# Performance work log

Hardware: AMD Instinct MI355X
Metric: run time of the kernel (lower is better)

## Reference

```python
import jax, jax.numpy as jnp
import numpy as np

B = 131072
N_X = 64
H = 512
LD = 8                      # latent_dim
N_THETA = 1 + LD + LD * (LD + 1) // 2   # 45
N_STEPS = 20
_IU = np.triu_indices(LD)   # static upper-tri index pairs for quadratic terms


def _layernorm(x, g, b, eps=1e-5):
    m = jnp.mean(x, axis=-1, keepdims=True)
    v = jnp.var(x, axis=-1, keepdims=True)
    return (x - m) * jax.lax.rsqrt(v + eps) * g + b


def _library(z):
    # Theta(z) = [1, z, upper-tri quadratic terms]  -> [B, N_THETA]
    ones = jnp.ones((z.shape[0], 1), z.dtype)
    quad = z[:, _IU[0]] * z[:, _IU[1]]
    return jnp.concatenate([ones, z, quad], axis=1)


def setup_inputs() -> dict:
    key = jax.random.key(0)
    ks = jax.random.split(key, 16)

    def W(k, fan_in, fan_out):
        # kaiming_normal (relu gain) as in the torch init
        return jax.random.normal(k, (fan_in, fan_out), jnp.float32) * np.sqrt(2.0 / fan_in)

    inp = {
        "x0_norm": jax.random.normal(ks[0], (B, N_X), jnp.float32),
        "log10_Dt_norm": jax.random.uniform(ks[1], (B, 1), jnp.float32),
        "Dt_mean": 0,
        "Dt_std": 1,
        # encoder: n_x -> 512 -> 512 -> latent (LN+SiLU between, final Tanh)
        "enc_W1": W(ks[2], N_X, H), "enc_b1": jnp.zeros((H,), jnp.float32),
        "enc_g1": jnp.ones((H,), jnp.float32), "enc_be1": jnp.zeros((H,), jnp.float32),
        "enc_W2": W(ks[3], H, H), "enc_b2": jnp.zeros((H,), jnp.float32),
        "enc_g2": jnp.ones((H,), jnp.float32), "enc_be2": jnp.zeros((H,), jnp.float32),
        "enc_W3": W(ks[4], H, LD), "enc_b3": jnp.zeros((LD,), jnp.float32),
        # decoder: latent -> 512 -> 512 -> n_x (LN+SiLU between, no final act)
        "dec_W1": W(ks[5], LD, H), "dec_b1": jnp.zeros((H,), jnp.float32),
        "dec_g1": jnp.ones((H,), jnp.float32), "dec_be1": jnp.zeros((H,), jnp.float32),
        "dec_W2": W(ks[6], H, H), "dec_b2": jnp.zeros((H,), jnp.float32),
        "dec_g2": jnp.ones((H,), jnp.float32), "dec_be2": jnp.zeros((H,), jnp.float32),
        "dec_W3": W(ks[7], H, N_X), "dec_b3": jnp.zeros((N_X,), jnp.float32),
        "Xi": 0.01 * jax.random.normal(ks[8], (N_THETA, LD), jnp.float32),
    }
    return inp


def reference(x0_norm, log10_Dt_norm, Dt_mean, Dt_std,
              enc_W1, enc_b1, enc_g1, enc_be1, enc_W2, enc_b2, enc_g2, enc_be2,
              enc_W3, enc_b3,
              dec_W1, dec_b1, dec_g1, dec_be1, dec_W2, dec_b2, dec_g2, dec_be2,
              dec_W3, dec_b3, Xi):
    # 1. encode: z0 = phi(x0)
    h = jax.nn.silu(_layernorm(x0_norm @ enc_W1 + enc_b1, enc_g1, enc_be1))
    h = jax.nn.silu(_layernorm(h @ enc_W2 + enc_b2, enc_g2, enc_be2))
    z0 = jnp.tanh(h @ enc_W3 + enc_b3)                       # [B, LD]

    # 2. Euler-integrate dz/dtau = Theta(z) Xi for N_STEPS fixed steps
    dt = log10_Dt_norm[:, :1] / N_STEPS                       # [B, 1]

    def step(z, _):
        zdot = _library(z) @ Xi                               # [B, LD]
        return z + zdot * dt, None

    z_t, _ = jax.lax.scan(step, z0, None, length=N_STEPS)

    # 3. decode: xhat = psi(z_t)
    h = jax.nn.silu(_layernorm(z_t @ dec_W1 + dec_b1, dec_g1, dec_be1))
    h = jax.nn.silu(_layernorm(h @ dec_W2 + dec_b2, dec_g2, dec_be2))
    xhat = h @ dec_W3 + dec_b3                                # [B, N_X]
    return xhat
```

## Files before the change

kernel.cpp:

```cpp
#include <hip/hip_runtime.h>
#include <hip/hip_bf16.h>
#include <math.h>

#define B_TOTAL 131072
#define NX 64
#define H 512
#define LD 8
#define NT 45
#define NSTEPS 20

#define NTH 512
#define BM 64
#define ASTR 520

#define OFF_EW1T 0
#define OFF_EW2T 32768
#define OFF_DW2T 294912
#define OFF_DW3T 557056
#define WS_ELEMS 589824
#define OFF_W3HI 589824
#define OFF_W3LO 598016
#define WS_ELEMS2 606208
#define OFF_DW1P 606208
#define WS_ELEMS3 622592
#define ZT_OFF_BYTES (WS_ELEMS3 * 2)
#define WS_NEW_BYTES (ZT_OFF_BYTES + (size_t)B_TOTAL * LD * 4)

typedef __attribute__((ext_vector_type(8))) short short8;
typedef __attribute__((ext_vector_type(4))) float f32x4;

__device__ __forceinline__ ushort f2bf(float f) {
    union { float f; uint u; } v; v.f = f;
    uint u = v.u;
    u += 0x7fff + ((u >> 16) & 1);
    return (ushort)(u >> 16);
}
__device__ __forceinline__ float bf2f(ushort s) {
    union { uint u; float f; } v; v.u = ((uint)s) << 16;
    return v.f;
}
__device__ __forceinline__ float silu_f(float v) {
    return v / (1.0f + __expf(-v));
}

__global__ void prep_weights(const float* __restrict__ eW1, const float* __restrict__ eW2,
                             const float* __restrict__ dW2, const float* __restrict__ dW3,
                             const float* __restrict__ eW3, const float* __restrict__ dW1,
                             short* __restrict__ ws) {
    const int id = blockIdx.x * 256 + threadIdx.x;
    if (id < OFF_EW2T) {
        const int kc = id >> 14, n = (id >> 5) & 511, kk = id & 31;
        ws[id] = (short)f2bf(eW1[(kc * 32 + kk) * H + n]);
    } else if (id < OFF_DW2T) {
        const int j = id - OFF_EW2T;
        const int kc = j >> 14, n = (j >> 5) & 511, kk = j & 31;
        ws[id] = (short)f2bf(eW2[(kc * 32 + kk) * H + n]);
    } else if (id < OFF_DW3T) {
        const int j = id - OFF_DW2T;
        const int kc = j >> 14, n = (j >> 5) & 511, kk = j & 31;
        ws[id] = (short)f2bf(dW2[(kc * 32 + kk) * H + n]);
    } else if (id < WS_ELEMS) {
        const int j = id - OFF_DW3T;
        const int kc = j >> 11, n = (j >> 5) & 63, kk = j & 31;
        ws[id] = (short)f2bf(dW3[(kc * 32 + kk) * NX + n]);
    } else if (id < OFF_W3LO) {
        const int j = id - OFF_W3HI, n = j >> 9, k = j & 511;
        const float v = (n < LD) ? eW3[k * LD + n] : 0.f;
        ws[id] = (short)f2bf(v);
    } else if (id < WS_ELEMS2) {
        const int j = id - OFF_W3LO, n = j >> 9, k = j & 511;
        const float v = (n < LD) ? eW3[k * LD + n] : 0.f;
        const float hi = bf2f(f2bf(v));
        ws[id] = (short)f2bf(v - hi);
    } else if (id < WS_ELEMS3) {
        const int j = id - OFF_DW1P;
        const int n = j >> 5, s = j & 31;
        const int k = s & 7;
        const float v = dW1[k * H + n];
        const ushort hi = f2bf(v);
        ws[id] = (((s >> 3) & 1) == 0) ? (short)hi : (short)f2bf(v - bf2f(hi));
    }
}

template <int K, int N>
__device__ __forceinline__ void gemm_chunked(const short (*act)[ASTR], const short* __restrict__ WTc,
                                             f32x4 (&acc)[4][4], int w, int lm, int q) {
    constexpr int NC = K / 32;
    constexpr int CS = N * 32;
    const short* bp = WTc + (w * 64 + lm) * 32 + q * 8;
#pragma unroll 1
    for (int kc = 0; kc < NC; ++kc) {
        short8 b[4];
        const short* p = bp + kc * CS;
#pragma unroll
        for (int tt = 0; tt < 4; ++tt) b[tt] = *(const short8*)(p + tt * 512);
        const int k0 = kc * 32 + q * 8;
#pragma unroll
        for (int mt = 0; mt < 4; ++mt) {
            short8 a = *(const short8*)&act[mt * 16 + lm][k0];
#pragma unroll
            for (int tt = 0; tt < 4; ++tt)
                acc[mt][tt] = __builtin_amdgcn_mfma_f32_16x16x32_bf16(a, b[tt], acc[mt][tt], 0, 0, 0);
        }
    }
}

__device__ __forceinline__ void ln_epi64(f32x4 (&acc)[4][4],
        const float* __restrict__ bias, const float* __restrict__ g, const float* __restrict__ be,
        short (*act)[ASTR], float (*p1)[8], float (*p2)[8], float (*rstat)[2],
        int w, int lane, int tid) {
    const int lm = lane & 15, q = lane >> 4;
    float cb[4], cg[4], cbe[4];
#pragma unroll
    for (int tt = 0; tt < 4; ++tt) {
        const int c = w * 64 + tt * 16 + lm;
        cb[tt] = bias[c]; cg[tt] = g[c]; cbe[tt] = be[c];
    }
#pragma unroll
    for (int mt = 0; mt < 4; ++mt) {
        float s1[4] = {0.f, 0.f, 0.f, 0.f}, s2[4] = {0.f, 0.f, 0.f, 0.f};
#pragma unroll
        for (int tt = 0; tt < 4; ++tt)
#pragma unroll
            for (int r = 0; r < 4; ++r) {
                float v = acc[mt][tt][r] + cb[tt];
                acc[mt][tt][r] = v;
                s1[r] += v;
                s2[r] += v * v;
            }
#pragma unroll
        for (int m = 1; m < 16; m <<= 1) {
#pragma unroll
            for (int r = 0; r < 4; ++r) {
                s1[r] += __shfl_xor(s1[r], m);
                s2[r] += __shfl_xor(s2[r], m);
            }
        }
        if (lm == 0) {
#pragma unroll
            for (int r = 0; r < 4; ++r) {
                const int row = mt * 16 + q * 4 + r;
                p1[row][w] = s1[r];
                p2[row][w] = s2[r];
            }
        }
    }
    __syncthreads();
    if (tid < BM) {
        float a = 0.f, b2 = 0.f;
#pragma unroll
        for (int j = 0; j < 8; ++j) { a += p1[tid][j]; b2 += p2[tid][j]; }
        const float mean = a * (1.0f / H);
        rstat[tid][0] = mean;
        rstat[tid][1] = rsqrtf(b2 * (1.0f / H) - mean * mean + 1e-5f);
    }
    __syncthreads();
#pragma unroll
    for (int mt = 0; mt < 4; ++mt) {
#pragma unroll
        for (int r = 0; r < 4; ++r) {
            const int row = mt * 16 + q * 4 + r;
            const float mu = rstat[row][0], rs = rstat[row][1];
#pragma unroll
            for (int tt = 0; tt < 4; ++tt) {
                const float v = (acc[mt][tt][r] - mu) * rs * cg[tt] + cbe[tt];
                act[row][w * 64 + tt * 16 + lm] = (short)f2bf(silu_f(v));
            }
        }
    }
    __syncthreads();
}

__global__ __launch_bounds__(NTH, 4) void sindy_enc_kernel(
        const float* __restrict__ x0, const float* __restrict__ logdt,
        const float* __restrict__ eb1, const float* __restrict__ eg1, const float* __restrict__ ebe1,
        const float* __restrict__ eb2, const float* __restrict__ eg2, const float* __restrict__ ebe2,
        const float* __restrict__ eb3, const float* __restrict__ Xi,
        const short* __restrict__ wsb, float* __restrict__ zt) {
    __shared__ __align__(16) short act[BM][ASTR];
    __shared__ __align__(16) float scratch[2048];
    __shared__ float rstat[BM][2];
    __shared__ float dtb[BM];
    __shared__ float xis[NT * LD];
    float (*p1)[8] = (float(*)[8])scratch;
    float (*p2)[8] = (float(*)[8])(scratch + 512);
    float (*partial)[BM][LD] = (float(*)[BM][LD])scratch;

    const int tid = threadIdx.x;
    const int w = tid >> 6, lane = tid & 63, lm = lane & 15, q = lane >> 4;
    const int row0 = blockIdx.x * BM;

    if (tid < NT * LD) xis[tid] = Xi[tid];
    if (tid < BM) dtb[tid] = logdt[row0 + tid] * (1.0f / NSTEPS);
    {
        const int r = tid >> 3, c8 = (tid & 7) * 8;
        const float* xr = &x0[(row0 + r) * NX + c8];
        const float4 va = *(const float4*)xr;
        const float4 vb = *(const float4*)(xr + 4);
        short8 sv;
        sv[0] = (short)f2bf(va.x); sv[1] = (short)f2bf(va.y);
        sv[2] = (short)f2bf(va.z); sv[3] = (short)f2bf(va.w);
        sv[4] = (short)f2bf(vb.x); sv[5] = (short)f2bf(vb.y);
        sv[6] = (short)f2bf(vb.z); sv[7] = (short)f2bf(vb.w);
        *(short8*)&act[r][c8] = sv;
    }
    __syncthreads();

    {
        f32x4 acc[4][4];
#pragma unroll
        for (int mt = 0; mt < 4; ++mt)
#pragma unroll
            for (int tt = 0; tt < 4; ++tt) acc[mt][tt] = (f32x4){0.f, 0.f, 0.f, 0.f};
        gemm_chunked<NX, H>(act, wsb + OFF_EW1T, acc, w, lm, q);
        ln_epi64(acc, eb1, eg1, ebe1, act, p1, p2, rstat, w, lane, tid);
    }

    {
        f32x4 acc[4][4];
#pragma unroll
        for (int mt = 0; mt < 4; ++mt)
#pragma unroll
            for (int tt = 0; tt < 4; ++tt) acc[mt][tt] = (f32x4){0.f, 0.f, 0.f, 0.f};
        gemm_chunked<H, H>(act, wsb + OFF_EW2T, acc, w, lm, q);
        ln_epi64(acc, eb2, eg2, ebe2, act, p1, p2, rstat, w, lane, tid);
    }

    float z0;
    {
        const short* W3H = wsb + OFF_W3HI;
        const short* W3L = wsb + OFF_W3LO;
        const int kq = w & 3, mh = w >> 2;
        f32x4 a3[2];
        a3[0] = (f32x4){0.f, 0.f, 0.f, 0.f};
        a3[1] = (f32x4){0.f, 0.f, 0.f, 0.f};
#pragma unroll
        for (int kc = 0; kc < 4; ++kc) {
            const int k0 = kq * 128 + kc * 32 + q * 8;
            short8 bh = *(const short8*)&W3H[lm * H + k0];
            short8 bl = *(const short8*)&W3L[lm * H + k0];
#pragma unroll
            for (int i = 0; i < 2; ++i) {
                short8 a = *(const short8*)&act[(mh * 2 + i) * 16 + lm][k0];
                a3[i] = __builtin_amdgcn_mfma_f32_16x16x32_bf16(a, bh, a3[i], 0, 0, 0);
                a3[i] = __builtin_amdgcn_mfma_f32_16x16x32_bf16(a, bl, a3[i], 0, 0, 0);
            }
        }
        if (lm < 8) {
#pragma unroll
            for (int i = 0; i < 2; ++i)
#pragma unroll
                for (int r = 0; r < 4; ++r)
                    partial[kq][(mh * 2 + i) * 16 + q * 4 + r][lm] = a3[i][r];
        }
        __syncthreads();
        {
            const int r = tid >> 3, c = tid & 7;
            const float s = partial[0][r][c] + partial[1][r][c] +
                            partial[2][r][c] + partial[3][r][c];
            z0 = tanhf(s + eb3[c]);
        }
    }

    {
        const int r = tid >> 3, c = tid & 7;
        const int lbase = lane & ~7;
        float xrl[1 + LD];
#pragma unroll
        for (int t = 0; t <= LD; ++t) xrl[t] = xis[t * LD + c];
        const float dtv = dtb[r];
        float zc = z0;
        for (int st = 0; st < NSTEPS; ++st) {
            float z[LD];
#pragma unroll
            for (int j = 0; j < LD; ++j) z[j] = __shfl(zc, lbase + j);
            float zd = xrl[0];
#pragma unroll
            for (int j = 0; j < LD; ++j) zd += z[j] * xrl[1 + j];
            int idx = 1 + LD;
#pragma unroll
            for (int i = 0; i < LD; ++i)
#pragma unroll
                for (int j = i; j < LD; ++j) {
                    zd += z[i] * z[j] * xis[idx * LD + c];
                    ++idx;
                }
            zc += zd * dtv;
        }
        zt[row0 * LD + tid] = zc;
    }
}

__global__ __launch_bounds__(NTH, 4) void sindy_dec_kernel(
        const float* __restrict__ zt,
        const float* __restrict__ db1,
        const float* __restrict__ dg1, const float* __restrict__ dbe1,
        const float* __restrict__ db2, const float* __restrict__ dg2, const float* __restrict__ dbe2,
        const float* __restrict__ db3,
        const short* __restrict__ wsb, float* __restrict__ out) {
    __shared__ __align__(16) short act[BM][ASTR];
    __shared__ float p1[BM][8], p2[BM][8], rstat[BM][2];
    __shared__ __align__(16) float zbuf[BM][LD];
    const int tid = threadIdx.x;
    const int w = tid >> 6, lane = tid & 63, lm = lane & 15, q = lane >> 4;
    const int row0 = blockIdx.x * BM;

    ((float*)zbuf)[tid] = zt[row0 * LD + tid];
    __syncthreads();

    {
        const short* bp = wsb + OFF_DW1P + (w * 64 + lm) * 32 + q * 8;
        short8 b[4];
#pragma unroll
        for (int tt = 0; tt < 4; ++tt) b[tt] = *(const short8*)(bp + tt * 512);
        f32x4 acc[4][4];
#pragma unroll
        for (int mt = 0; mt < 4; ++mt) {
            const int row = mt * 16 + lm;
            const float4 za = *(const float4*)&zbuf[row][0];
            const float4 zb = *(const float4*)&zbuf[row][4];
            float zv[LD] = {za.x, za.y, za.z, za.w, zb.x, zb.y, zb.z, zb.w};
            short8 a;
#pragma unroll
            for (int j = 0; j < LD; ++j) {
                const ushort h = f2bf(zv[j]);
                a[j] = (q < 2) ? (short)h : (short)f2bf(zv[j] - bf2f(h));
            }
#pragma unroll
            for (int tt = 0; tt < 4; ++tt)
                acc[mt][tt] = __builtin_amdgcn_mfma_f32_16x16x32_bf16(
                    a, b[tt], (f32x4){0.f, 0.f, 0.f, 0.f}, 0, 0, 0);
        }
        ln_epi64(acc, db1, dg1, dbe1, act, p1, p2, rstat, w, lane, tid);
    }

    {
        f32x4 acc[4][4];
#pragma unroll
        for (int mt = 0; mt < 4; ++mt)
#pragma unroll
            for (int tt = 0; tt < 4; ++tt) acc[mt][tt] = (f32x4){0.f, 0.f, 0.f, 0.f};
        gemm_chunked<H, H>(act, wsb + OFF_DW2T, acc, w, lm, q);
        ln_epi64(acc, db2, dg2, dbe2, act, p1, p2, rstat, w, lane, tid);
    }

    {
        const short* W3c = wsb + OFF_DW3T;
        const int nt = w & 3, mtb = (w >> 2) << 1;
        const short* bp = W3c + (nt * 16 + lm) * 32 + q * 8;
        f32x4 a2[2];
        a2[0] = (f32x4){0.f, 0.f, 0.f, 0.f};
        a2[1] = (f32x4){0.f, 0.f, 0.f, 0.f};
#pragma unroll 1
        for (int kc = 0; kc < 16; ++kc) {
            short8 b = *(const short8*)(bp + kc * 2048);
            const int k0 = kc * 32 + q * 8;
#pragma unroll
            for (int i = 0; i < 2; ++i) {
                short8 a = *(const short8*)&act[(mtb + i) * 16 + lm][k0];
                a2[i] = __builtin_amdgcn_mfma_f32_16x16x32_bf16(a, b, a2[i], 0, 0, 0);
            }
        }
        const int c = nt * 16 + lm;
        const float bb = db3[c];
#pragma unroll
        for (int i = 0; i < 2; ++i)
#pragma unroll
            for (int r = 0; r < 4; ++r) {
                const int row = (mtb + i) * 16 + q * 4 + r;
                out[(row0 + row) * NX + c] = a2[i][r] + bb;
            }
    }
}

#define FB_R 16
#define FB_STRIDE 520
#define FB_NT 256

__device__ __forceinline__ void fb_ln_silu(float buf[FB_R][FB_STRIDE],
                                           const float* __restrict__ g,
                                           const float* __restrict__ be, int t) {
    const int r = t >> 4, lane = t & 15;
    float s1 = 0.f, s2 = 0.f;
#pragma unroll
    for (int j = 0; j < H / 16; ++j) {
        float v = buf[r][lane + 16 * j];
        s1 += v; s2 += v * v;
    }
#pragma unroll
    for (int m = 8; m >= 1; m >>= 1) {
        s1 += __shfl_xor(s1, m, 16);
        s2 += __shfl_xor(s2, m, 16);
    }
    const float mean = s1 * (1.0f / H);
    const float var = s2 * (1.0f / H) - mean * mean;
    const float rstd = rsqrtf(var + 1e-5f);
#pragma unroll
    for (int j = 0; j < H / 16; ++j) {
        const int c = lane + 16 * j;
        float v = buf[r][c];
        buf[r][c] = silu_f((v - mean) * rstd * g[c] + be[c]);
    }
}

template <int K>
__device__ __forceinline__ void fb_gemmK(const float in[FB_R][FB_STRIDE], float out[FB_R][FB_STRIDE],
                                         const float* __restrict__ W,
                                         const float* __restrict__ b, int t) {
    const int c0 = t, c1 = t + 256;
    float acc0[FB_R], acc1[FB_R];
#pragma unroll
    for (int r = 0; r < FB_R; ++r) { acc0[r] = 0.f; acc1[r] = 0.f; }
    for (int k = 0; k < K; k += 4) {
        const float w00 = W[(k + 0) * H + c0], w10 = W[(k + 0) * H + c1];
        const float w01 = W[(k + 1) * H + c0], w11 = W[(k + 1) * H + c1];
        const float w02 = W[(k + 2) * H + c0], w12 = W[(k + 2) * H + c1];
        const float w03 = W[(k + 3) * H + c0], w13 = W[(k + 3) * H + c1];
#pragma unroll
        for (int r = 0; r < FB_R; ++r) {
            const float4 h = *(const float4*)&in[r][k];
            acc0[r] += h.x * w00 + h.y * w01 + h.z * w02 + h.w * w03;
            acc1[r] += h.x * w10 + h.y * w11 + h.z * w12 + h.w * w13;
        }
    }
    const float b0 = b[c0], b1 = b[c1];
#pragma unroll
    for (int r = 0; r < FB_R; ++r) {
        out[r][c0] = acc0[r] + b0;
        out[r][c1] = acc1[r] + b1;
    }
}

__global__ __launch_bounds__(FB_NT, 2) void sindy_fallback_kernel(
    const float* __restrict__ x0, const float* __restrict__ logdt,
    const float* __restrict__ eW1, const float* __restrict__ eb1,
    const float* __restrict__ eg1, const float* __restrict__ ebe1,
    const float* __restrict__ eW2, const float* __restrict__ eb2,
    const float* __restrict__ eg2, const float* __restrict__ ebe2,
    const float* __restrict__ eW3, const float* __restrict__ eb3,
    const float* __restrict__ dW1, const float* __restrict__ db1,
    const float* __restrict__ dg1, const float* __restrict__ dbe1,
    const float* __restrict__ dW2, const float* __restrict__ db2,
    const float* __restrict__ dg2, const float* __restrict__ dbe2,
    const float* __restrict__ dW3, const float* __restrict__ db3,
    const float* __restrict__ Xi, float* __restrict__ out) {
    __shared__ float sA[FB_R][FB_STRIDE];
    __shared__ float sB[FB_R][FB_STRIDE];
    __shared__ float zbuf[FB_R][LD];
    __shared__ float dtb[FB_R];
    __shared__ float xis[NT * LD];

    const int t = threadIdx.x;
    const int row0 = blockIdx.x * FB_R;

    for (int i = t; i < NT * LD; i += FB_NT) xis[i] = Xi[i];
    if (t < FB_R) dtb[t] = logdt[row0 + t] * (1.0f / NSTEPS);
    {
        const int r = t >> 4, k4 = (t & 15) * 4;
        *(float4*)&sB[r][k4] = *(const float4*)&x0[(row0 + r) * NX + k4];
    }
    __syncthreads();
    fb_gemmK<NX>(sB, sA, eW1, eb1, t);
    __syncthreads();
    fb_ln_silu(sA, eg1, ebe1, t);
    __syncthreads();
    fb_gemmK<H>(sA, sB, eW2, eb2, t);
    __syncthreads();
    fb_ln_silu(sB, eg2, ebe2, t);
    __syncthreads();
    if (t < FB_R * LD) {
        const int r = t >> 3, c = t & 7;
        float acc = 0.f;
        for (int k = 0; k < H; k += 4) {
            const float4 h = *(const float4*)&sB[r][k];
            acc += h.x * eW3[(k + 0) * LD + c] + h.y * eW3[(k + 1) * LD + c] +
                   h.z * eW3[(k + 2) * LD + c] + h.w * eW3[(k + 3) * LD + c];
        }
        zbuf[r][c] = tanhf(acc + eb3[c]);
    }
    __syncthreads();
    for (int s = 0; s < NSTEPS; ++s) {
        float zn = 0.f;
        const int r = t >> 3, c = t & 7;
        if (t < FB_R * LD) {
            float z[LD];
#pragma unroll
            for (int j = 0; j < LD; ++j) z[j] = zbuf[r][j];
            float zd = xis[c];
#pragma unroll
            for (int j = 0; j < LD; ++j) zd += z[j] * xis[(1 + j) * LD + c];
            int idx = 1 + LD;
#pragma unroll
            for (int i = 0; i < LD; ++i)
#pragma unroll
                for (int j = i; j < LD; ++j) {
                    zd += z[i] * z[j] * xis[idx * LD + c];
                    ++idx;
                }
            zn = z[c] + zd * dtb[r];
        }
        __syncthreads();
        if (t < FB_R * LD) zbuf[r][c] = zn;
        __syncthreads();
    }
    {
        const int c0 = t, c1 = t + 256;
        float acc0[FB_R], acc1[FB_R];
#pragma unroll
        for (int r = 0; r < FB_R; ++r) { acc0[r] = 0.f; acc1[r] = 0.f; }
#pragma unroll
        for (int k = 0; k < LD; ++k) {
            const float w0 = dW1[k * H + c0], w1 = dW1[k * H + c1];
#pragma unroll
            for (int r = 0; r < FB_R; ++r) {
                const float zv = zbuf[r][k];
                acc0[r] += zv * w0;
                acc1[r] += zv * w1;
            }
        }
        const float b0 = db1[c0], b1v = db1[c1];
#pragma unroll
        for (int r = 0; r < FB_R; ++r) {
            sA[r][c0] = acc0[r] + b0;
            sA[r][c1] = acc1[r] + b1v;
        }
    }
    __syncthreads();
    fb_ln_silu(sA, dg1, dbe1, t);
    __syncthreads();
    fb_gemmK<H>(sA, sB, dW2, db2, t);
    __syncthreads();
    fb_ln_silu(sB, dg2, dbe2, t);
    __syncthreads();
    {
        const int c = t & 63;
        const int rb = t >> 6;
        float acc[4] = {0.f, 0.f, 0.f, 0.f};
        for (int k = 0; k < H; k += 4) {
            const float w0 = dW3[(k + 0) * NX + c];
            const float w1 = dW3[(k + 1) * NX + c];
            const float w2 = dW3[(k + 2) * NX + c];
            const float w3 = dW3[(k + 3) * NX + c];
#pragma unroll
            for (int i = 0; i < 4; ++i) {
                const int r = rb + 4 * i;
                const float4 h = *(const float4*)&sB[r][k];
                acc[i] += h.x * w0 + h.y * w1 + h.z * w2 + h.w * w3;
            }
        }
        const float bb = db3[c];
#pragma unroll
        for (int i = 0; i < 4; ++i) {
            const int r = rb + 4 * i;
            out[(row0 + r) * NX + c] = acc[i] + bb;
        }
    }
}

extern "C" void kernel_launch(void* const* d_in, const int* in_sizes, int n_in,
                              void* d_out, int out_size, void* d_ws, size_t ws_size,
                              hipStream_t stream) {
    const float* x0    = (const float*)d_in[0];
    const float* logdt = (const float*)d_in[1];
    const float* eW1  = (const float*)d_in[4];
    const float* eb1  = (const float*)d_in[5];
    const float* eg1  = (const float*)d_in[6];
    const float* ebe1 = (const float*)d_in[7];
    const float* eW2  = (const float*)d_in[8];
    const float* eb2  = (const float*)d_in[9];
    const float* eg2  = (const float*)d_in[10];
    const float* ebe2 = (const float*)d_in[11];
    const float* eW3  = (const float*)d_in[12];
    const float* eb3  = (const float*)d_in[13];
    const float* dW1  = (const float*)d_in[14];
    const float* db1  = (const float*)d_in[15];
    const float* dg1  = (const float*)d_in[16];
    const float* dbe1 = (const float*)d_in[17];
    const float* dW2  = (const float*)d_in[18];
    const float* db2  = (const float*)d_in[19];
    const float* dg2  = (const float*)d_in[20];
    const float* dbe2 = (const float*)d_in[21];
    const float* dW3  = (const float*)d_in[22];
    const float* db3  = (const float*)d_in[23];
    const float* Xi   = (const float*)d_in[24];
    float* out = (float*)d_out;

    if (ws_size >= WS_NEW_BYTES) {
        short* wsb = (short*)d_ws;
        float* zt = (float*)((char*)d_ws + ZT_OFF_BYTES);
        prep_weights<<<WS_ELEMS3 / 256, 256, 0, stream>>>(eW1, eW2, dW2, dW3, eW3, dW1, wsb);
        sindy_enc_kernel<<<B_TOTAL / BM, NTH, 0, stream>>>(
            x0, logdt, eb1, eg1, ebe1, eb2, eg2, ebe2, eb3, Xi, wsb, zt);
        sindy_dec_kernel<<<B_TOTAL / BM, NTH, 0, stream>>>(
            zt, db1, dg1, dbe1, db2, dg2, dbe2, db3, wsb, out);
    } else {
        sindy_fallback_kernel<<<B_TOTAL / FB_R, FB_NT, 0, stream>>>(
            x0, logdt, eW1, eb1, eg1, ebe1, eW2, eb2, eg2, ebe2, eW3, eb3,
            dW1, db1, dg1, dbe1, dW2, db2, dg2, dbe2, dW3, db3, Xi, out);
    }
}
```

Measured before the change: 469.4 us.

## Stage 512x512 GEMM weights through padded LDS with async global_load_lds double-buffering

The hidden-layer 512x512 weights are repacked into a padded row layout (stride 40 shorts) and streamed per wave into a double-buffered LDS slice using global_load_lds. Each k-chunk is prefetched while the previous one feeds the MFMAs. This replaces direct global short8 loads of B fragments and is meant to hide load latency and avoid LDS bank conflicts. The LDS footprint grows, so launch bounds drop from 4 to 2 blocks per SM, which lowers occupancy. The Euler loop also caches all 45 Xi coefficients in registers instead of reading them from LDS.

```diff
diff --git a/kernel.cpp b/kernel.cpp
--- a/kernel.cpp
+++ b/kernel.cpp
@@ -13,17 +13,19 @@
 #define BM 64
 #define ASTR 520
 
+#define BROW 40
+#define BSLICE 2560
+#define BCH 20480
+
 #define OFF_EW1T 0
-#define OFF_EW2T 32768
-#define OFF_DW2T 294912
-#define OFF_DW3T 557056
-#define WS_ELEMS 589824
-#define OFF_W3HI 589824
-#define OFF_W3LO 598016
-#define WS_ELEMS2 606208
-#define OFF_DW1P 606208
-#define WS_ELEMS3 622592
-#define ZT_OFF_BYTES (WS_ELEMS3 * 2)
+#define OFF_EW2P 32768
+#define OFF_DW2P 360448
+#define OFF_DW3T 688128
+#define OFF_W3HI 720896
+#define OFF_W3LO 729088
+#define OFF_DW1P 737280
+#define WS_ALL   753664
+#define ZT_OFF_BYTES ((size_t)WS_ALL * 2)
 #define WS_NEW_BYTES (ZT_OFF_BYTES + (size_t)B_TOTAL * LD * 4)
 
 typedef __attribute__((ext_vector_type(8))) short short8;
@@ -48,18 +50,18 @@
                              const float* __restrict__ eW3, const float* __restrict__ dW1,
                              short* __restrict__ ws) {
     const int id = blockIdx.x * 256 + threadIdx.x;
-    if (id < OFF_EW2T) {
+    if (id < OFF_EW2P) {
         const int kc = id >> 14, n = (id >> 5) & 511, kk = id & 31;
         ws[id] = (short)f2bf(eW1[(kc * 32 + kk) * H + n]);
-    } else if (id < OFF_DW2T) {
-        const int j = id - OFF_EW2T;
-        const int kc = j >> 14, n = (j >> 5) & 511, kk = j & 31;
-        ws[id] = (short)f2bf(eW2[(kc * 32 + kk) * H + n]);
+    } else if (id < OFF_DW2P) {
+        const int j = id - OFF_EW2P;
+        const int kc = j / BCH, rm = j % BCH, n = rm / BROW, s = rm % BROW;
+        ws[id] = (s < 32) ? (short)f2bf(eW2[(kc * 32 + s) * H + n]) : (short)0;
     } else if (id < OFF_DW3T) {
-        const int j = id - OFF_DW2T;
-        const int kc = j >> 14, n = (j >> 5) & 511, kk = j & 31;
-        ws[id] = (short)f2bf(dW2[(kc * 32 + kk) * H + n]);
-    } else if (id < WS_ELEMS) {
+        const int j = id - OFF_DW2P;
+        const int kc = j / BCH, rm = j % BCH, n = rm / BROW, s = rm % BROW;
+        ws[id] = (s < 32) ? (short)f2bf(dW2[(kc * 32 + s) * H + n]) : (short)0;
+    } else if (id < OFF_W3HI) {
         const int j = id - OFF_DW3T;
         const int kc = j >> 11, n = (j >> 5) & 63, kk = j & 31;
         ws[id] = (short)f2bf(dW3[(kc * 32 + kk) * NX + n]);
@@ -67,12 +69,12 @@
         const int j = id - OFF_W3HI, n = j >> 9, k = j & 511;
         const float v = (n < LD) ? eW3[k * LD + n] : 0.f;
         ws[id] = (short)f2bf(v);
-    } else if (id < WS_ELEMS2) {
+    } else if (id < OFF_DW1P) {
         const int j = id - OFF_W3LO, n = j >> 9, k = j & 511;
         const float v = (n < LD) ? eW3[k * LD + n] : 0.f;
         const float hi = bf2f(f2bf(v));
         ws[id] = (short)f2bf(v - hi);
-    } else if (id < WS_ELEMS3) {
+    } else if (id < WS_ALL) {
         const int j = id - OFF_DW1P;
         const int n = j >> 5, s = j & 31;
         const int k = s & 7;
@@ -82,16 +84,56 @@
     }
 }
 
-template <int K, int N>
-__device__ __forceinline__ void gemm_chunked(const short (*act)[ASTR], const short* __restrict__ WTc,
-                                             f32x4 (&acc)[4][4], int w, int lm, int q) {
-    constexpr int NC = K / 32;
-    constexpr int CS = N * 32;
+__device__ __forceinline__ void load_lds16(const void* g, void* l) {
+    __builtin_amdgcn_global_load_lds(
+        (const __attribute__((address_space(1))) void*)g,
+        (__attribute__((address_space(3))) void*)l, 16, 0, 0);
+}
+
+__device__ __forceinline__ void stage_slice(const short* __restrict__ gsrc, short* ldst, int lane) {
+#pragma unroll
+    for (int j = 0; j < 5; ++j) {
+        const int off = j * 1024 + lane * 16;
+        load_lds16((const char*)gsrc + off, (char*)ldst + off);
+    }
+}
+
+__device__ __forceinline__ void gemm_lds512(const short (*act)[ASTR], const short* __restrict__ WP,
+                                            short* bwave, f32x4 (&acc)[4][4],
+                                            int w, int lane, int lm, int q) {
+    const short* gbase = WP + w * BSLICE;
+    stage_slice(gbase, bwave, lane);
+#pragma unroll 1
+    for (int kc = 0; kc < 16; ++kc) {
+        if (kc + 1 < 16) {
+            stage_slice(gbase + (kc + 1) * BCH, bwave + ((kc + 1) & 1) * BSLICE, lane);
+            asm volatile("s_waitcnt vmcnt(5)" ::: "memory");
+        } else {
+            asm volatile("s_waitcnt vmcnt(0)" ::: "memory");
+        }
+        const short* bb = bwave + (kc & 1) * BSLICE;
+        short8 b[4];
+#pragma unroll
+        for (int tt = 0; tt < 4; ++tt)
+            b[tt] = *(const short8*)(bb + (tt * 16 + lm) * BROW + q * 8);
+        const int k0 = kc * 32 + q * 8;
+#pragma unroll
+        for (int mt = 0; mt < 4; ++mt) {
+            short8 a = *(const short8*)&act[mt * 16 + lm][k0];
+#pragma unroll
+            for (int tt = 0; tt < 4; ++tt)
+                acc[mt][tt] = __builtin_amdgcn_mfma_f32_16x16x32_bf16(a, b[tt], acc[mt][tt], 0, 0, 0);
+        }
+    }
+}
+
+__device__ __forceinline__ void gemm_direct64(const short (*act)[ASTR], const short* __restrict__ WTc,
+                                              f32x4 (&acc)[4][4], int w, int lm, int q) {
     const short* bp = WTc + (w * 64 + lm) * 32 + q * 8;
 #pragma unroll 1
-    for (int kc = 0; kc < NC; ++kc) {
+    for (int kc = 0; kc < 2; ++kc) {
         short8 b[4];
-        const short* p = bp + kc * CS;
+        const short* p = bp + kc * (H * 32);
 #pragma unroll
         for (int tt = 0; tt < 4; ++tt) b[tt] = *(const short8*)(p + tt * 512);
         const int k0 = kc * 32 + q * 8;
@@ -171,24 +213,25 @@
     __syncthreads();
 }
 
-__global__ __launch_bounds__(NTH, 4) void sindy_enc_kernel(
+__global__ __launch_bounds__(NTH, 2) void sindy_enc_kernel(
         const float* __restrict__ x0, const float* __restrict__ logdt,
         const float* __restrict__ eb1, const float* __restrict__ eg1, const float* __restrict__ ebe1,
         const float* __restrict__ eb2, const float* __restrict__ eg2, const float* __restrict__ ebe2,
         const float* __restrict__ eb3, const float* __restrict__ Xi,
         const short* __restrict__ wsb, float* __restrict__ zt) {
     __shared__ __align__(16) short act[BM][ASTR];
-    __shared__ __align__(16) float scratch[2048];
+    __shared__ __align__(16) short bbuf[8 * 2 * BSLICE];
     __shared__ float rstat[BM][2];
     __shared__ float dtb[BM];
     __shared__ float xis[NT * LD];
-    float (*p1)[8] = (float(*)[8])scratch;
-    float (*p2)[8] = (float(*)[8])(scratch + 512);
-    float (*partial)[BM][LD] = (float(*)[BM][LD])scratch;
+    float (*p1)[8] = (float(*)[8])bbuf;
+    float (*p2)[8] = (float(*)[8])(bbuf + 1024);
+    float (*partial)[BM][LD] = (float(*)[BM][LD])bbuf;
 
     const int tid = threadIdx.x;
     const int w = tid >> 6, lane = tid & 63, lm = lane & 15, q = lane >> 4;
     const int row0 = blockIdx.x * BM;
+    short* bwave = bbuf + w * 2 * BSLICE;
 
     if (tid < NT * LD) xis[tid] = Xi[tid];
     if (tid < BM) dtb[tid] = logdt[row0 + tid] * (1.0f / NSTEPS);
@@ -212,7 +255,7 @@
         for (int mt = 0; mt < 4; ++mt)
 #pragma unroll
             for (int tt = 0; tt < 4; ++tt) acc[mt][tt] = (f32x4){0.f, 0.f, 0.f, 0.f};
-        gemm_chunked<NX, H>(act, wsb + OFF_EW1T, acc, w, lm, q);
+        gemm_direct64(act, wsb + OFF_EW1T, acc, w, lm, q);
         ln_epi64(acc, eb1, eg1, ebe1, act, p1, p2, rstat, w, lane, tid);
     }
 
@@ -222,7 +265,7 @@
         for (int mt = 0; mt < 4; ++mt)
 #pragma unroll
             for (int tt = 0; tt < 4; ++tt) acc[mt][tt] = (f32x4){0.f, 0.f, 0.f, 0.f};
-        gemm_chunked<H, H>(act, wsb + OFF_EW2T, acc, w, lm, q);
+        gemm_lds512(act, wsb + OFF_EW2P, bwave, acc, w, lane, lm, q);
         ln_epi64(acc, eb2, eg2, ebe2, act, p1, p2, rstat, w, lane, tid);
     }
 
@@ -265,24 +308,24 @@
     {
         const int r = tid >> 3, c = tid & 7;
         const int lbase = lane & ~7;
-        float xrl[1 + LD];
-#pragma unroll
-        for (int t = 0; t <= LD; ++t) xrl[t] = xis[t * LD + c];
+        float xr[NT];
+#pragma unroll
+        for (int t = 0; t < NT; ++t) xr[t] = xis[t * LD + c];
         const float dtv = dtb[r];
         float zc = z0;
         for (int st = 0; st < NSTEPS; ++st) {
             float z[LD];
 #pragma unroll
             for (int j = 0; j < LD; ++j) z[j] = __shfl(zc, lbase + j);
-            float zd = xrl[0];
-#pragma unroll
-            for (int j = 0; j < LD; ++j) zd += z[j] * xrl[1 + j];
+            float zd = xr[0];
+#pragma unroll
+            for (int j = 0; j < LD; ++j) zd += z[j] * xr[1 + j];
             int idx = 1 + LD;
 #pragma unroll
             for (int i = 0; i < LD; ++i)
 #pragma unroll
                 for (int j = i; j < LD; ++j) {
-                    zd += z[i] * z[j] * xis[idx * LD + c];
+                    zd += z[i] * z[j] * xr[idx];
                     ++idx;
                 }
             zc += zd * dtv;
@@ -291,7 +334,7 @@
     }
 }
 
-__global__ __launch_bounds__(NTH, 4) void sindy_dec_kernel(
+__global__ __launch_bounds__(NTH, 2) void sindy_dec_kernel(
         const float* __restrict__ zt,
         const float* __restrict__ db1,
         const float* __restrict__ dg1, const float* __restrict__ dbe1,
@@ -299,11 +342,16 @@
         const float* __restrict__ db3,
         const short* __restrict__ wsb, float* __restrict__ out) {
     __shared__ __align__(16) short act[BM][ASTR];
-    __shared__ float p1[BM][8], p2[BM][8], rstat[BM][2];
+    __shared__ __align__(16) short bbuf[8 * 2 * BSLICE];
+    __shared__ float rstat[BM][2];
     __shared__ __align__(16) float zbuf[BM][LD];
+    float (*p1)[8] = (float(*)[8])bbuf;
+    float (*p2)[8] = (float(*)[8])(bbuf + 1024);
+
     const int tid = threadIdx.x;
     const int w = tid >> 6, lane = tid & 63, lm = lane & 15, q = lane >> 4;
     const int row0 = blockIdx.x * BM;
+    short* bwave = bbuf + w * 2 * BSLICE;
 
     ((float*)zbuf)[tid] = zt[row0 * LD + tid];
     __syncthreads();
@@ -340,7 +388,7 @@
         for (int mt = 0; mt < 4; ++mt)
 #pragma unroll
             for (int tt = 0; tt < 4; ++tt) acc[mt][tt] = (f32x4){0.f, 0.f, 0.f, 0.f};
-        gemm_chunked<H, H>(act, wsb + OFF_DW2T, acc, w, lm, q);
+        gemm_lds512(act, wsb + OFF_DW2P, bwave, acc, w, lane, lm, q);
         ln_epi64(acc, db2, dg2, dbe2, act, p1, p2, rstat, w, lane, tid);
     }
 
@@ -588,7 +636,7 @@
     if (ws_size >= WS_NEW_BYTES) {
         short* wsb = (short*)d_ws;
         float* zt = (float*)((char*)d_ws + ZT_OFF_BYTES);
-        prep_weights<<<WS_ELEMS3 / 256, 256, 0, stream>>>(eW1, eW2, dW2, dW3, eW3, dW1, wsb);
+        prep_weights<<<WS_ALL / 256, 256, 0, stream>>>(eW1, eW2, dW2, dW3, eW3, dW1, wsb);
         sindy_enc_kernel<<<B_TOTAL / BM, NTH, 0, stream>>>(
             x0, logdt, eb1, eg1, ebe1, eb2, eg2, ebe2, eb3, Xi, wsb, zt);
         sindy_dec_kernel<<<B_TOTAL / BM, NTH, 0, stream>>>(
```

Result: slower. 604.3 us (+28.7%).
